# Performance work log

Hardware: AMD Instinct MI355X
Metric: run time of the kernel (lower is better)

## Reference

```python
import jax, jax.numpy as jnp
import numpy as np

B, T, E, H = 2, 2048, 1024, 16
D = E // H
K_KEEP = 391
RECENCY = 64
SCALE = D ** -0.5


def setup_inputs() -> dict:
    key = jax.random.key(0)
    k1, k2, k3 = jax.random.split(key, 3)
    x = jax.random.normal(k1, (B, T, E), jnp.float32)
    W_attn = jax.random.normal(k2, (3 * E, E), jnp.float32) * 0.02  # torch Linear weight [out,in]
    W_proj = jax.random.normal(k3, (E, E), jnp.float32) * 0.02
    return {"x": x, "W_attn": W_attn, "W_proj": W_proj}


def reference(x, W_attn, W_proj):
    b, t, c = x.shape
    qkv = x @ W_attn.T                      # [B,T,3E]
    q, k, v = jnp.split(qkv, 3, axis=-1)
    to_heads = lambda u: u.reshape(b, t, H, D).transpose(0, 2, 1, 3)  # [B,H,T,D]
    q, k, v = to_heads(q), to_heads(k), to_heads(v)

    # first pass: causal attention weights for importance scoring
    scores = jnp.einsum('bhqd,bhkd->bhqk', q, k) * SCALE
    causal = jnp.tril(jnp.ones((t, t), dtype=bool))
    scores = jnp.where(causal, scores, -jnp.inf)
    attn_w = jax.nn.softmax(scores, axis=-1)

    # mean importance over query dim, force-keep recent tokens
    imp = attn_w.mean(axis=2)               # [B,H,T]
    imp = imp.at[:, :, -RECENCY:].set(1.0)

    # top-k token selection per (batch, head)
    _, idx = jax.lax.top_k(imp, K_KEEP)     # [B,H,K]

    # gather pruned K/V
    K_keep = jnp.take_along_axis(k, idx[..., None], axis=2)  # [B,H,K,D]
    V_keep = jnp.take_along_axis(v, idx[..., None], axis=2)

    # second attention pass over pruned keys (no causal mask, matches legacy code)
    s2 = jnp.einsum('bhqd,bhkd->bhqk', q, K_keep) * SCALE
    a2 = jax.nn.softmax(s2, axis=-1)
    out = jnp.einsum('bhqk,bhkd->bhqd', a2, V_keep)          # [B,H,T,D]

    out = out.transpose(0, 2, 1, 3).reshape(b, t, c)
    return out @ W_proj.T
```

## Files before the change

### kernel.cpp

```cpp
#include <hip/hip_runtime.h>
#include <hip/hip_bf16.h>


#define TT 2048
#define EE 1024
#define HH 16
#define DD 64
#define KKEEP 391
#define REC 64
#define NBH 32
#define QSCALE 0.125f
#define KPAD 448

typedef short bf16x8 __attribute__((ext_vector_type(8)));
typedef _Float16 f16x8 __attribute__((ext_vector_type(8)));
typedef float f32x4 __attribute__((ext_vector_type(4)));

static __device__ inline unsigned short bf_rn(float x) {
  unsigned u = __float_as_uint(x);
  unsigned r = u + 0x7fffu + ((u >> 16) & 1u);
  return (unsigned short)(r >> 16);
}
static __device__ inline float bf_up(unsigned short h) {
  return __uint_as_float((unsigned)h << 16);
}
static __device__ inline unsigned pkf16(float a, float b) {
  union { _Float16 h[2]; unsigned u; } t;
  t.h[0] = (_Float16)a; t.h[1] = (_Float16)b; return t.u;
}
static __device__ inline void glds16(const void* g, void* l) {
  __builtin_amdgcn_global_load_lds(
      (const __attribute__((address_space(1))) void*)g,
      (__attribute__((address_space(3))) void*)l, 16, 0, 0);
}

__global__ __launch_bounds__(256) void split_kernel(
    const float* __restrict__ src, unsigned short* __restrict__ ho,
    unsigned short* __restrict__ lo_, int n)
{
  int i = (blockIdx.x * 256 + threadIdx.x) * 4;
  const int stride = gridDim.x * 1024;
  for (; i < n; i += stride) {
    float4 v = *reinterpret_cast<const float4*>(&src[i]);
    ushort4 hh, ll;
    float f;
    hh.x = bf_rn(v.x); f = bf_up(hh.x); ll.x = bf_rn(v.x - f);
    hh.y = bf_rn(v.y); f = bf_up(hh.y); ll.y = bf_rn(v.y - f);
    hh.z = bf_rn(v.z); f = bf_up(hh.z); ll.z = bf_rn(v.z - f);
    hh.w = bf_rn(v.w); f = bf_up(hh.w); ll.w = bf_rn(v.w - f);
    *reinterpret_cast<ushort4*>(&ho[i]) = hh;
    *reinterpret_cast<ushort4*>(&lo_[i]) = ll;
  }
}

__global__ __launch_bounds__(256) void gemm_bf16s_nt(
    const unsigned short* __restrict__ Ah, const unsigned short* __restrict__ Al,
    const unsigned short* __restrict__ Bh, const unsigned short* __restrict__ Bl,
    float* __restrict__ Cc, unsigned short* __restrict__ Qho, unsigned short* __restrict__ Qlo,
    unsigned short* __restrict__ Kho, unsigned short* __restrict__ Klo,
    float* __restrict__ Vo, int M, int N, int Kd, int mode)
{
  __shared__ __align__(16) unsigned short Ahs[2][128 * 32];
  __shared__ __align__(16) unsigned short Als[2][128 * 32];
  __shared__ __align__(16) unsigned short Bhs[2][128 * 32];
  __shared__ __align__(16) unsigned short Bls[2][128 * 32];
  const int tid = threadIdx.x;
  const int m0 = blockIdx.y * 128, n0 = blockIdx.x * 128;
  const int w = tid >> 6, lane = tid & 63;
  const int wm = w >> 1, wn = w & 1;
  const int l15 = lane & 15, l4 = lane >> 4;
  const bool vblk = (mode == 1) && (blockIdx.x >= 16);

  size_t gA[2], gB[2]; int ldso[2];
#pragma unroll
  for (int s = 0; s < 2; s++) {
    int seg = w * 2 + s;
    int r = seg * 16 + (lane >> 2);
    int kb = (lane & 3) ^ ((r >> 1) & 3);
    gA[s] = (size_t)(m0 + r) * Kd + kb * 8;
    gB[s] = (size_t)(n0 + r) * Kd + kb * 8;
    ldso[s] = seg * 512;
  }

  auto STAGE = [&](int bb, int k0) {
#pragma unroll
    for (int s = 0; s < 2; s++) {
      glds16(&Ah[gA[s] + k0], &Ahs[bb][ldso[s]]);
      glds16(&Bh[gB[s] + k0], &Bhs[bb][ldso[s]]);
      if (!vblk) {
        glds16(&Al[gA[s] + k0], &Als[bb][ldso[s]]);
        glds16(&Bl[gB[s] + k0], &Bls[bb][ldso[s]]);
      }
    }
  };

  f32x4 acc[4][4] = {};

  STAGE(0, 0);
  __syncthreads();
  int cur = 0;
  for (int k0 = 0; k0 < Kd; k0 += 32) {
    if (k0 + 32 < Kd) STAGE(cur ^ 1, k0 + 32);
    bf16x8 ah[4], al[4], bh[4], bl[4];
#pragma unroll
    for (int i = 0; i < 4; i++) {
      int ar = wm * 64 + i * 16 + l15;
      int aoff = ar * 32 + ((l4 ^ ((ar >> 1) & 3)) * 8);
      ah[i] = *reinterpret_cast<const bf16x8*>(&Ahs[cur][aoff]);
      int br = wn * 64 + i * 16 + l15;
      int boff = br * 32 + ((l4 ^ ((br >> 1) & 3)) * 8);
      bh[i] = *reinterpret_cast<const bf16x8*>(&Bhs[cur][boff]);
      if (!vblk) {
        al[i] = *reinterpret_cast<const bf16x8*>(&Als[cur][aoff]);
        bl[i] = *reinterpret_cast<const bf16x8*>(&Bls[cur][boff]);
      }
    }
#pragma unroll
    for (int i = 0; i < 4; i++)
#pragma unroll
      for (int j = 0; j < 4; j++) {
        acc[i][j] = __builtin_amdgcn_mfma_f32_16x16x32_bf16(ah[i], bh[j], acc[i][j], 0, 0, 0);
        if (!vblk) {
          acc[i][j] = __builtin_amdgcn_mfma_f32_16x16x32_bf16(ah[i], bl[j], acc[i][j], 0, 0, 0);
          acc[i][j] = __builtin_amdgcn_mfma_f32_16x16x32_bf16(al[i], bh[j], acc[i][j], 0, 0, 0);
        }
      }
    __syncthreads();
    cur ^= 1;
  }

  if (mode == 0) {
#pragma unroll
    for (int i = 0; i < 4; i++) {
      int mrow0 = m0 + wm * 64 + i * 16 + l4 * 4;
#pragma unroll
      for (int j = 0; j < 4; j++) {
        int ncol = n0 + wn * 64 + j * 16 + l15;
#pragma unroll
        for (int r = 0; r < 4; r++)
          Cc[(size_t)(mrow0 + r) * N + ncol] = acc[i][j][r];
      }
    }
  } else {
#pragma unroll
    for (int j = 0; j < 4; j++) {
      int n = n0 + wn * 64 + j * 16 + l15;
      int p = n >> 10, rr = n & 1023;
      int h = rr >> 6, d0 = rr & 63;
#pragma unroll
      for (int i = 0; i < 4; i++) {
        int mrow0 = m0 + wm * 64 + i * 16 + l4 * 4;
#pragma unroll
        for (int r = 0; r < 4; r++) {
          int m = mrow0 + r;
          int b = m >> 11, t = m & 2047;
          size_t idx = ((size_t)((b * HH + h) * TT + t)) * DD + d0;
          float v = acc[i][j][r];
          if (p == 2) {
            Vo[idx] = v;
          } else {
            unsigned short hi_ = bf_rn(v);
            unsigned short lo2 = bf_rn(v - bf_up(hi_));
            if (p == 0) { Qho[idx] = hi_; Qlo[idx] = lo2; }
            else        { Kho[idx] = hi_; Klo[idx] = lo2; }
          }
        }
      }
    }
  }
}

__global__ __launch_bounds__(512) void importance3_kernel(
    const unsigned short* __restrict__ Qh, const unsigned short* __restrict__ Ql,
    const unsigned short* __restrict__ Kh, const unsigned short* __restrict__ Kl,
    float* __restrict__ part)
{
  const int pairid = blockIdx.y, bh = blockIdx.x;
  const int tid = threadIdx.x;
  const int w = tid >> 6, lane = tid & 63;
  const int wm = w >> 1, wn = w & 1;
  const int l15 = lane & 15, l4 = lane >> 4;
  __shared__ __align__(16) unsigned short Qhs[128 * 64];
  __shared__ __align__(16) unsigned short Qls[128 * 64];
  __shared__ __align__(16) unsigned short Khs[2][128 * 64];
  __shared__ __align__(16) unsigned short Kls[2][128 * 64];
  __shared__ float csw[8 * 128];
  __shared__ float rsb[2 * 128];

  int krow[2], kkb[2], klds[2];
#pragma unroll
  for (int s = 0; s < 2; s++) {
    int seg = w * 2 + s;
    int r = seg * 8 + (lane >> 3);
    int k8 = lane & 7;
    krow[s] = r; kkb[s] = k8 ^ (r & 7); klds[s] = seg * 512;
  }
  auto STAGEK = [&](int bb, int ci) {
#pragma unroll
    for (int s = 0; s < 2; s++) {
      size_t ga = ((size_t)(bh * TT + ci * 128 + krow[s])) * DD + kkb[s] * 8;
      glds16(&Kh[ga], &Khs[bb][klds[s]]);
      glds16(&Kl[ga], &Kls[bb][klds[s]]);
    }
  };

  for (int half = 0; half < 2; half++) {
    const int rt = half ? (15 - pairid) : pairid;
    const int row0 = rt * 128;
    const int nch = rt + 1;
    __syncthreads();
#pragma unroll
    for (int cc = 0; cc < 2; cc++) {
      int c = cc * 512 + tid;
      int r = c >> 3, k8 = c & 7;
      int so = r * 64 + ((k8 ^ (r & 7)) * 8);
      size_t ga = ((size_t)(bh * TT + row0 + r)) * DD + k8 * 8;
      *reinterpret_cast<bf16x8*>(&Qhs[so]) = *reinterpret_cast<const bf16x8*>(&Qh[ga]);
      *reinterpret_cast<bf16x8*>(&Qls[so]) = *reinterpret_cast<const bf16x8*>(&Ql[ga]);
    }

    float rsum[2][4];
#pragma unroll
    for (int i = 0; i < 2; i++)
#pragma unroll
      for (int r = 0; r < 4; r++) rsum[i][r] = 0.f;
    float invl[2][4];

    for (int sweep = 0; sweep < 2; sweep++) {
      STAGEK(0, 0);
      __syncthreads();
      int cur = 0;
      for (int ci = 0; ci < nch; ci++) {
        if (ci + 1 < nch) STAGEK(cur ^ 1, ci + 1);
        f32x4 acc[2][4] = {};
#pragma unroll
        for (int ks = 0; ks < 2; ks++) {
          bf16x8 ah[2], al_[2];
#pragma unroll
          for (int i = 0; i < 2; i++) {
            int ar = wm * 32 + i * 16 + l15;
            int off = ar * 64 + (((ks * 4 + l4) ^ (ar & 7)) * 8);
            ah[i]  = *reinterpret_cast<const bf16x8*>(&Qhs[off]);
            al_[i] = *reinterpret_cast<const bf16x8*>(&Qls[off]);
          }
#pragma unroll
          for (int j = 0; j < 4; j++) {
            int br = wn * 64 + j * 16 + l15;
            int off = br * 64 + (((ks * 4 + l4) ^ (br & 7)) * 8);
            bf16x8 bh_ = *reinterpret_cast<const bf16x8*>(&Khs[cur][off]);
            bf16x8 bl_ = *reinterpret_cast<const bf16x8*>(&Kls[cur][off]);
#pragma unroll
            for (int i = 0; i < 2; i++) {
              acc[i][j] = __builtin_amdgcn_mfma_f32_16x16x32_bf16(ah[i], bh_, acc[i][j], 0, 0, 0);
              acc[i][j] = __builtin_amdgcn_mfma_f32_16x16x32_bf16(ah[i], bl_, acc[i][j], 0, 0, 0);
              acc[i][j] = __builtin_amdgcn_mfma_f32_16x16x32_bf16(al_[i], bh_, acc[i][j], 0, 0, 0);
            }
          }
        }
        const bool diag = (ci == rt);
        if (sweep == 0) {
#pragma unroll
          for (int i = 0; i < 2; i++)
#pragma unroll
            for (int r = 0; r < 4; r++) {
              int row = row0 + wm * 32 + i * 16 + l4 * 4 + r;
              float s = 0.f;
#pragma unroll
              for (int j = 0; j < 4; j++) {
                int key = ci * 128 + wn * 64 + j * 16 + l15;
                float p = __expf(acc[i][j][r] * QSCALE);
                if (diag && key > row) p = 0.f;
                s += p;
              }
              rsum[i][r] += s;
            }
          __syncthreads();
        } else {
          float cp[4];
#pragma unroll
          for (int j = 0; j < 4; j++) cp[j] = 0.f;
#pragma unroll
          for (int i = 0; i < 2; i++)
#pragma unroll
            for (int r = 0; r < 4; r++) {
              int row = row0 + wm * 32 + i * 16 + l4 * 4 + r;
              float il = invl[i][r];
#pragma unroll
              for (int j = 0; j < 4; j++) {
                int key = ci * 128 + wn * 64 + j * 16 + l15;
                float p = __expf(acc[i][j][r] * QSCALE) * il;
                if (diag && key > row) p = 0.f;
                cp[j] += p;
              }
            }
#pragma unroll
          for (int j = 0; j < 4; j++) {
            float v = cp[j];
            v += __shfl_xor(v, 16); v += __shfl_xor(v, 32);
            cp[j] = v;
          }
          if (l4 == 0) {
#pragma unroll
            for (int j = 0; j < 4; j++)
              csw[w * 128 + wn * 64 + j * 16 + l15] = cp[j];
          }
          __syncthreads();
          if (tid < 128) {
            int wnc = tid >> 6;
            float s = csw[(0 * 2 + wnc) * 128 + tid] + csw[(1 * 2 + wnc) * 128 + tid] +
                      csw[(2 * 2 + wnc) * 128 + tid] + csw[(3 * 2 + wnc) * 128 + tid];
            size_t pi = ((size_t)(bh * 8 + pairid)) * 2048 + ci * 128 + tid;
            bool wr = (half == 0) || (ci > pairid);
            part[pi] = wr ? s : (part[pi] + s);
          }
          __syncthreads();
        }
        cur ^= 1;
      }
      if (sweep == 0) {
#pragma unroll
        for (int i = 0; i < 2; i++)
#pragma unroll
          for (int r = 0; r < 4; r++) {
            float v = rsum[i][r];
            v += __shfl_xor(v, 1); v += __shfl_xor(v, 2);
            v += __shfl_xor(v, 4); v += __shfl_xor(v, 8);
            rsum[i][r] = v;
          }
        if (l15 == 0) {
#pragma unroll
          for (int i = 0; i < 2; i++)
#pragma unroll
            for (int r = 0; r < 4; r++)
              rsb[wn * 128 + wm * 32 + i * 16 + l4 * 4 + r] = rsum[i][r];
        }
        __syncthreads();
#pragma unroll
        for (int i = 0; i < 2; i++)
#pragma unroll
          for (int r = 0; r < 4; r++) {
            int rl = wm * 32 + i * 16 + l4 * 4 + r;
            invl[i][r] = 1.0f / (rsb[rl] + rsb[128 + rl]);
          }
      }
    }
  }
}

__global__ __launch_bounds__(256) void topk_gather_kernel(
    const float* __restrict__ part,
    const unsigned short* __restrict__ Kh, const unsigned short* __restrict__ Kl,
    const float* __restrict__ V,
    unsigned short* __restrict__ Kf, unsigned short* __restrict__ Vt)
{
  const int bh = blockIdx.x, tid = threadIdx.x;
  const int lane = tid & 63, w = tid >> 6;
  __shared__ int redi[4];
  __shared__ int stot;
  __shared__ int base[256];
  __shared__ int idxb[KKEEP];
  unsigned u[8];
#pragma unroll
  for (int k = 0; k < 8; k++) {
    int e = tid * 8 + k;
    float s = 0.f;
#pragma unroll
    for (int p = 0; p < 8; p++)
      if (e < (16 - p) * 128) s += part[((size_t)(bh * 8 + p)) * 2048 + e];
    float v = (e >= TT - REC) ? 3.0e3f : s;
    u[k] = __float_as_uint(v);
  }
  unsigned lo = 0u, hi = 0x7f800000u;
  for (int it = 0; it < 31; it++) {
    unsigned mid = lo + ((hi - lo + 1) >> 1);
    int c = 0;
#pragma unroll
    for (int k = 0; k < 8; k++) c += (u[k] >= mid) ? 1 : 0;
#pragma unroll
    for (int off = 1; off <= 32; off <<= 1) c += __shfl_xor(c, off);
    if (lane == 0) redi[w] = c;
    __syncthreads();
    int tot = redi[0] + redi[1] + redi[2] + redi[3];
    if (tot >= KKEEP) lo = mid; else hi = mid - 1;
    __syncthreads();
  }
  const unsigned vstar = lo;
  int cgt = 0, ceq = 0;
#pragma unroll
  for (int k = 0; k < 8; k++) { cgt += (u[k] > vstar) ? 1 : 0; ceq += (u[k] == vstar) ? 1 : 0; }
  base[tid] = cgt; __syncthreads();
  if (tid == 0) {
    int run = 0;
    for (int i = 0; i < 256; i++) { int t = base[i]; base[i] = run; run += t; }
    stot = run;
  }
  __syncthreads();
  int off1 = base[tid];
#pragma unroll
  for (int k = 0; k < 8; k++)
    if (u[k] > vstar) idxb[off1++] = tid * 8 + k;
  __syncthreads();
  base[tid] = ceq; __syncthreads();
  if (tid == 0) {
    int run = 0;
    for (int i = 0; i < 256; i++) { int t = base[i]; base[i] = run; run += t; }
  }
  __syncthreads();
  int off2 = stot + base[tid];
#pragma unroll
  for (int k = 0; k < 8; k++)
    if (u[k] == vstar) { if (off2 < KKEEP) idxb[off2] = tid * 8 + k; off2++; }
  __syncthreads();
  for (int f = tid; f < KPAD * 8; f += 256) {
    int kk = f >> 3, c8 = f & 7;
    union { _Float16 h[8]; uint4 v; } o;
#pragma unroll
    for (int j = 0; j < 8; j++) o.h[j] = (_Float16)0.f;
    if (kk < KKEEP) {
      int sr = idxb[kk];
      bf16x8 hv = *reinterpret_cast<const bf16x8*>(&Kh[((size_t)(bh * TT + sr)) * DD + c8 * 8]);
      bf16x8 lv = *reinterpret_cast<const bf16x8*>(&Kl[((size_t)(bh * TT + sr)) * DD + c8 * 8]);
#pragma unroll
      for (int j = 0; j < 8; j++)
        o.h[j] = (_Float16)(bf_up((unsigned short)hv[j]) + bf_up((unsigned short)lv[j]));
    }
    *reinterpret_cast<uint4*>(&Kf[((size_t)(bh * KPAD) + kk) * DD + c8 * 8]) = o.v;
  }
  for (int f = tid; f < KPAD * 8; f += 256) {
    int kk = f >> 3, d8 = f & 7;
    float vv[8];
#pragma unroll
    for (int j = 0; j < 8; j++) vv[j] = 0.f;
    if (kk < KKEEP) {
      int sr = idxb[kk];
      float4 a = *reinterpret_cast<const float4*>(&V[((size_t)(bh * TT + sr)) * DD + d8 * 8]);
      float4 b = *reinterpret_cast<const float4*>(&V[((size_t)(bh * TT + sr)) * DD + d8 * 8 + 4]);
      vv[0] = a.x; vv[1] = a.y; vv[2] = a.z; vv[3] = a.w;
      vv[4] = b.x; vv[5] = b.y; vv[6] = b.z; vv[7] = b.w;
    }
#pragma unroll
    for (int j = 0; j < 8; j++) {
      union { _Float16 h; unsigned short s; } t;
      t.h = (_Float16)vv[j];
      Vt[((size_t)(bh * DD) + d8 * 8 + j) * KPAD + kk] = t.s;
    }
  }
}

__global__ __launch_bounds__(256) void attn3_kernel(
    const unsigned short* __restrict__ Qh, const unsigned short* __restrict__ Ql,
    const unsigned short* __restrict__ Kf, const unsigned short* __restrict__ Vt,
    unsigned short* __restrict__ AOh, unsigned short* __restrict__ AOl)
{
  const int rt = blockIdx.y, bh = blockIdx.x;
  const int tid = threadIdx.x;
  const int w = tid >> 6, lane = tid & 63;
  const int l15 = lane & 15, l4 = lane >> 4;
  __shared__ __align__(16) unsigned short Qs[64 * 64];
  __shared__ __align__(16) unsigned short Ks[2][64 * 64];
  __shared__ __align__(16) unsigned short Vs[2][64 * 64];
  __shared__ float LDSo[4][64][16];
  const int row0 = rt * 64;

  int srow[2], skb[2], slds[2];
#pragma unroll
  for (int s = 0; s < 2; s++) {
    int seg = w * 2 + s;
    int r = seg * 8 + (lane >> 3);
    int k8 = lane & 7;
    srow[s] = r; skb[s] = k8 ^ (r & 7); slds[s] = seg * 512;
  }
  auto STAGEA = [&](int bb, int ci) {
#pragma unroll
    for (int s = 0; s < 2; s++) {
      glds16(&Kf[((size_t)(bh * KPAD) + ci * 64 + srow[s]) * DD + skb[s] * 8], &Ks[bb][slds[s]]);
      glds16(&Vt[((size_t)(bh * DD) + srow[s]) * KPAD + ci * 64 + skb[s] * 8], &Vs[bb][slds[s]]);
    }
  };

#pragma unroll
  for (int it = 0; it < 2; it++) {
    int idx = it * 256 + tid;
    int r = idx >> 3, k8 = idx & 7;
    size_t ga = ((size_t)(bh * TT + row0 + r)) * DD + k8 * 8;
    bf16x8 hv = *reinterpret_cast<const bf16x8*>(&Qh[ga]);
    bf16x8 lv = *reinterpret_cast<const bf16x8*>(&Ql[ga]);
    union { _Float16 h[8]; uint4 v; } q16;
#pragma unroll
    for (int j = 0; j < 8; j++)
      q16.h[j] = (_Float16)(bf_up((unsigned short)hv[j]) + bf_up((unsigned short)lv[j]));
    *reinterpret_cast<uint4*>(&Qs[r * 64 + ((k8 ^ (r & 7)) * 8)]) = q16.v;
  }
  STAGEA(0, 0);
  __syncthreads();
  f16x8 bq[2];
#pragma unroll
  for (int ks = 0; ks < 2; ks++) {
    int br = w * 16 + l15;
    bq[ks] = *reinterpret_cast<const f16x8*>(&Qs[br * 64 + (((ks * 4 + l4) ^ (br & 7)) * 8)]);
  }

  f32x4 acc_o[4] = {};
  float rsum = 0.f;
  int cur = 0;

  for (int ci = 0; ci < 7; ci++) {
    if (ci + 1 < 7) STAGEA(cur ^ 1, ci + 1);
    f32x4 accs[4] = {};
#pragma unroll
    for (int ks = 0; ks < 2; ks++) {
#pragma unroll
      for (int i = 0; i < 4; i++) {
        int kr = i * 16 + l15;
        f16x8 af = *reinterpret_cast<const f16x8*>(&Ks[cur][kr * 64 + (((ks * 4 + l4) ^ (kr & 7)) * 8)]);
        accs[i] = __builtin_amdgcn_mfma_f32_16x16x32_f16(af, bq[ks], accs[i], 0, 0, 0);
      }
    }
    float p[4][4];
#pragma unroll
    for (int i = 0; i < 4; i++)
#pragma unroll
      for (int r = 0; r < 4; r++) {
        int gk = ci * 64 + i * 16 + l4 * 4 + r;
        float pp = __expf(accs[i][r] * QSCALE);
        if (gk >= KKEEP) pp = 0.f;
        p[i][r] = pp;
        rsum += pp;
      }
    unsigned pkU[4][2];
#pragma unroll
    for (int i = 0; i < 4; i++) {
      pkU[i][0] = pkf16(p[i][0], p[i][1]);
      pkU[i][1] = pkf16(p[i][2], p[i][3]);
    }
#pragma unroll
    for (int ks = 0; ks < 2; ks++) {
      union { f16x8 h; unsigned u[4]; } bp;
#pragma unroll
      for (int wp = 0; wp < 4; wp++) {
        int src = ((l4 & 1) * 2 + (wp >> 1)) * 16 + l15;
        unsigned v0 = (unsigned)__shfl((int)pkU[ks * 2][wp & 1], src);
        unsigned v1 = (unsigned)__shfl((int)pkU[ks * 2 + 1][wp & 1], src);
        bp.u[wp] = (l4 & 2) ? v1 : v0;
      }
#pragma unroll
      for (int i = 0; i < 4; i++) {
        int dr = i * 16 + l15;
        f16x8 av = *reinterpret_cast<const f16x8*>(&Vs[cur][dr * 64 + (((ks * 4 + l4) ^ (dr & 7)) * 8)]);
        acc_o[i] = __builtin_amdgcn_mfma_f32_16x16x32_f16(av, bp.h, acc_o[i], 0, 0, 0);
      }
    }
    __syncthreads();
    cur ^= 1;
  }
  rsum += __shfl_xor(rsum, 16);
  rsum += __shfl_xor(rsum, 32);
  float inv = 1.0f / rsum;
#pragma unroll
  for (int i = 0; i < 4; i++)
#pragma unroll
    for (int r = 0; r < 4; r++)
      LDSo[w][i * 16 + l4 * 4 + r][l15] = acc_o[i][r] * inv;
  __syncthreads();
  const int b = bh >> 4, h = bh & 15;
#pragma unroll
  for (int uu = 0; uu < 2; uu++) {
    int u = uu * 64 + lane;
    int q = u >> 3, dc = u & 7;
    int row = row0 + w * 16 + q;
    union { unsigned short s[8]; uint4 v; } sh, sl;
#pragma unroll
    for (int j = 0; j < 8; j++) {
      float v = LDSo[w][dc * 8 + j][q];
      unsigned short hh = bf_rn(v);
      sh.s[j] = hh;
      sl.s[j] = bf_rn(v - bf_up(hh));
    }
    size_t addr = ((size_t)(b * TT + row)) * EE + h * DD + dc * 8;
    *reinterpret_cast<uint4*>(&AOh[addr]) = sh.v;
    *reinterpret_cast<uint4*>(&AOl[addr]) = sl.v;
  }
}

extern "C" void kernel_launch(void* const* d_in, const int* in_sizes, int n_in,
                              void* d_out, int out_size, void* d_ws, size_t ws_size,
                              hipStream_t stream)
{
  const float* x     = (const float*)d_in[0];
  const float* Wattn = (const float*)d_in[1];
  const float* Wproj = (const float*)d_in[2];
  float* out = (float*)d_out;
  float* ws  = (float*)d_ws;

  const size_t SZQ = (size_t)NBH * TT * DD;
  const size_t SZK = (size_t)NBH * KPAD * DD;
  float* Vb   = ws;
  float* part = Vb + SZQ;
  unsigned short* Kf  = (unsigned short*)(part + (size_t)NBH * 8 * TT);
  unsigned short* Vt  = Kf + SZK;
  unsigned short* Qhp = Vt + SZK;
  unsigned short* Qlp = Qhp + SZQ;
  unsigned short* Khp = Qlp + SZQ;
  unsigned short* Klp = Khp + SZQ;
  unsigned short* xh  = Klp + SZQ;
  unsigned short* xl  = xh + (size_t)4096 * 1024;
  unsigned short* Wh  = xl + (size_t)4096 * 1024;
  unsigned short* Wl  = Wh + (size_t)3072 * 1024;
  unsigned short* AOh = xh;
  unsigned short* AOl = xl;
  unsigned short* Ph  = Wh;
  unsigned short* Pl  = Ph + (size_t)1024 * 1024;

  const size_t needB =
      ((size_t)SZQ + (size_t)NBH * 8 * TT) * 4 +
      ((size_t)2 * SZK + (size_t)4 * SZQ + (size_t)2 * 4096 * 1024 + (size_t)2 * 3072 * 1024) * 2;
  if (ws_size < needB) return;

  split_kernel<<<512, 256, 0, stream>>>(x, xh, xl, 4096 * 1024);
  split_kernel<<<512, 256, 0, stream>>>(Wattn, Wh, Wl, 3072 * 1024);
  gemm_bf16s_nt<<<dim3(24, 32), 256, 0, stream>>>(xh, xl, Wh, Wl, nullptr,
                                                  Qhp, Qlp, Khp, Klp, Vb, 4096, 3072, 1024, 1);
  split_kernel<<<512, 256, 0, stream>>>(Wproj, Ph, Pl, 1024 * 1024);
  importance3_kernel<<<dim3(NBH, 8), 512, 0, stream>>>(Qhp, Qlp, Khp, Klp, part);
  topk_gather_kernel<<<NBH, 256, 0, stream>>>(part, Khp, Klp, Vb, Kf, Vt);
  attn3_kernel<<<dim3(NBH, 32), 256, 0, stream>>>(Qhp, Qlp, Kf, Vt, AOh, AOl);
  gemm_bf16s_nt<<<dim3(8, 32), 256, 0, stream>>>(AOh, AOl, Ph, Pl, out,
                                                 nullptr, nullptr, nullptr, nullptr, nullptr,
                                                 4096, 1024, 1024, 0);
}
```

Before: 313.3 us.

## Deepen async-copy pipelines, split QKV GEMM by V precision, fuse split launches

```diff
diff --git a/kernel.cpp b/kernel.cpp
--- a/kernel.cpp
+++ b/kernel.cpp
@@ -16,6 +16,10 @@
 typedef _Float16 f16x8 __attribute__((ext_vector_type(8)));
 typedef float f32x4 __attribute__((ext_vector_type(4)));
 
+#define WAIT_VM(N) asm volatile("s_waitcnt vmcnt(" #N ")" ::: "memory")
+#define WAIT_LGKM0 asm volatile("s_waitcnt lgkmcnt(0)" ::: "memory")
+#define BAR() __builtin_amdgcn_s_barrier()
+
 static __device__ inline unsigned short bf_rn(float x) {
   unsigned u = __float_as_uint(x);
   unsigned r = u + 0x7fffu + ((u >> 16) & 1u);
@@ -34,42 +38,61 @@
       (__attribute__((address_space(3))) void*)l, 16, 0, 0);
 }
 
+static __device__ inline void split4(const float* __restrict__ src,
+                                     unsigned short* __restrict__ ho,
+                                     unsigned short* __restrict__ lo_, int i)
+{
+  float4 v = *reinterpret_cast<const float4*>(&src[i]);
+  ushort4 hh, ll;
+  float f;
+  hh.x = bf_rn(v.x); f = bf_up(hh.x); ll.x = bf_rn(v.x - f);
+  hh.y = bf_rn(v.y); f = bf_up(hh.y); ll.y = bf_rn(v.y - f);
+  hh.z = bf_rn(v.z); f = bf_up(hh.z); ll.z = bf_rn(v.z - f);
+  hh.w = bf_rn(v.w); f = bf_up(hh.w); ll.w = bf_rn(v.w - f);
+  *reinterpret_cast<ushort4*>(&ho[i]) = hh;
+  *reinterpret_cast<ushort4*>(&lo_[i]) = ll;
+}
+
 __global__ __launch_bounds__(256) void split_kernel(
     const float* __restrict__ src, unsigned short* __restrict__ ho,
     unsigned short* __restrict__ lo_, int n)
 {
   int i = (blockIdx.x * 256 + threadIdx.x) * 4;
   const int stride = gridDim.x * 1024;
-  for (; i < n; i += stride) {
-    float4 v = *reinterpret_cast<const float4*>(&src[i]);
-    ushort4 hh, ll;
-    float f;
-    hh.x = bf_rn(v.x); f = bf_up(hh.x); ll.x = bf_rn(v.x - f);
-    hh.y = bf_rn(v.y); f = bf_up(hh.y); ll.y = bf_rn(v.y - f);
-    hh.z = bf_rn(v.z); f = bf_up(hh.z); ll.z = bf_rn(v.z - f);
-    hh.w = bf_rn(v.w); f = bf_up(hh.w); ll.w = bf_rn(v.w - f);
-    *reinterpret_cast<ushort4*>(&ho[i]) = hh;
-    *reinterpret_cast<ushort4*>(&lo_[i]) = ll;
-  }
-}
-
-__global__ __launch_bounds__(256) void gemm_bf16s_nt(
+  for (; i < n; i += stride) split4(src, ho, lo_, i);
+}
+
+__global__ __launch_bounds__(256) void split2_kernel(
+    const float* __restrict__ x, const float* __restrict__ wa,
+    unsigned short* __restrict__ xh, unsigned short* __restrict__ xl,
+    unsigned short* __restrict__ wh, unsigned short* __restrict__ wl)
+{
+  const int n1 = 4096 * 1024, n2 = 3072 * 1024;
+  int i = (blockIdx.x * 256 + threadIdx.x) * 4;
+  const int stride = gridDim.x * 1024;
+  for (; i < n1 + n2; i += stride) {
+    if (i < n1) split4(x, xh, xl, i);
+    else        split4(wa, wh, wl, i - n1);
+  }
+}
+
+template<bool VB, int MODE>
+__global__ __launch_bounds__(256) void gemm_pipe(
     const unsigned short* __restrict__ Ah, const unsigned short* __restrict__ Al,
     const unsigned short* __restrict__ Bh, const unsigned short* __restrict__ Bl,
     float* __restrict__ Cc, unsigned short* __restrict__ Qho, unsigned short* __restrict__ Qlo,
     unsigned short* __restrict__ Kho, unsigned short* __restrict__ Klo,
-    float* __restrict__ Vo, int M, int N, int Kd, int mode)
+    float* __restrict__ Vo, int M, int N, int Kd, int nOff)
 {
   __shared__ __align__(16) unsigned short Ahs[2][128 * 32];
-  __shared__ __align__(16) unsigned short Als[2][128 * 32];
   __shared__ __align__(16) unsigned short Bhs[2][128 * 32];
-  __shared__ __align__(16) unsigned short Bls[2][128 * 32];
+  __shared__ __align__(16) unsigned short Als[VB ? 1 : 2][128 * 32];
+  __shared__ __align__(16) unsigned short Bls[VB ? 1 : 2][128 * 32];
   const int tid = threadIdx.x;
-  const int m0 = blockIdx.y * 128, n0 = blockIdx.x * 128;
+  const int m0 = blockIdx.y * 128, n0 = nOff + blockIdx.x * 128;
   const int w = tid >> 6, lane = tid & 63;
   const int wm = w >> 1, wn = w & 1;
   const int l15 = lane & 15, l4 = lane >> 4;
-  const bool vblk = (mode == 1) && (blockIdx.x >= 16);
 
   size_t gA[2], gB[2]; int ldso[2];
 #pragma unroll
@@ -81,13 +104,12 @@
     gB[s] = (size_t)(n0 + r) * Kd + kb * 8;
     ldso[s] = seg * 512;
   }
-
   auto STAGE = [&](int bb, int k0) {
 #pragma unroll
     for (int s = 0; s < 2; s++) {
       glds16(&Ah[gA[s] + k0], &Ahs[bb][ldso[s]]);
       glds16(&Bh[gB[s] + k0], &Bhs[bb][ldso[s]]);
-      if (!vblk) {
+      if (!VB) {
         glds16(&Al[gA[s] + k0], &Als[bb][ldso[s]]);
         glds16(&Bl[gB[s] + k0], &Bls[bb][ldso[s]]);
       }
@@ -97,10 +119,12 @@
   f32x4 acc[4][4] = {};
 
   STAGE(0, 0);
-  __syncthreads();
+  STAGE(1, 32);
   int cur = 0;
   for (int k0 = 0; k0 < Kd; k0 += 32) {
-    if (k0 + 32 < Kd) STAGE(cur ^ 1, k0 + 32);
+    if (k0 + 32 < Kd) { if (VB) WAIT_VM(4); else WAIT_VM(8); }
+    else WAIT_VM(0);
+    BAR();
     bf16x8 ah[4], al[4], bh[4], bl[4];
 #pragma unroll
     for (int i = 0; i < 4; i++) {
@@ -110,7 +134,7 @@
       int br = wn * 64 + i * 16 + l15;
       int boff = br * 32 + ((l4 ^ ((br >> 1) & 3)) * 8);
       bh[i] = *reinterpret_cast<const bf16x8*>(&Bhs[cur][boff]);
-      if (!vblk) {
+      if (!VB) {
         al[i] = *reinterpret_cast<const bf16x8*>(&Als[cur][aoff]);
         bl[i] = *reinterpret_cast<const bf16x8*>(&Bls[cur][boff]);
       }
@@ -120,16 +144,18 @@
 #pragma unroll
       for (int j = 0; j < 4; j++) {
         acc[i][j] = __builtin_amdgcn_mfma_f32_16x16x32_bf16(ah[i], bh[j], acc[i][j], 0, 0, 0);
-        if (!vblk) {
+        if (!VB) {
           acc[i][j] = __builtin_amdgcn_mfma_f32_16x16x32_bf16(ah[i], bl[j], acc[i][j], 0, 0, 0);
           acc[i][j] = __builtin_amdgcn_mfma_f32_16x16x32_bf16(al[i], bh[j], acc[i][j], 0, 0, 0);
         }
       }
-    __syncthreads();
+    WAIT_LGKM0;
+    BAR();
+    if (k0 + 64 < Kd) STAGE(cur, k0 + 64);
     cur ^= 1;
   }
 
-  if (mode == 0) {
+  if (MODE == 0) {
 #pragma unroll
     for (int i = 0; i < 4; i++) {
       int mrow0 = m0 + wm * 64 + i * 16 + l4 * 4;
@@ -139,6 +165,23 @@
 #pragma unroll
         for (int r = 0; r < 4; r++)
           Cc[(size_t)(mrow0 + r) * N + ncol] = acc[i][j][r];
+      }
+    }
+  } else if (VB) {
+#pragma unroll
+    for (int j = 0; j < 4; j++) {
+      int n = n0 + wn * 64 + j * 16 + l15;
+      int rr = n & 1023;
+      int h = rr >> 6, d0 = rr & 63;
+#pragma unroll
+      for (int i = 0; i < 4; i++) {
+        int mrow0 = m0 + wm * 64 + i * 16 + l4 * 4;
+#pragma unroll
+        for (int r = 0; r < 4; r++) {
+          int m = mrow0 + r;
+          int b = m >> 11, t = m & 2047;
+          Vo[((size_t)((b * HH + h) * TT + t)) * DD + d0] = acc[i][j][r];
+        }
       }
     }
   } else {
@@ -156,21 +199,17 @@
           int b = m >> 11, t = m & 2047;
           size_t idx = ((size_t)((b * HH + h) * TT + t)) * DD + d0;
           float v = acc[i][j][r];
-          if (p == 2) {
-            Vo[idx] = v;
-          } else {
-            unsigned short hi_ = bf_rn(v);
-            unsigned short lo2 = bf_rn(v - bf_up(hi_));
-            if (p == 0) { Qho[idx] = hi_; Qlo[idx] = lo2; }
-            else        { Kho[idx] = hi_; Klo[idx] = lo2; }
-          }
+          unsigned short hi_ = bf_rn(v);
+          unsigned short lo2 = bf_rn(v - bf_up(hi_));
+          if (p == 0) { Qho[idx] = hi_; Qlo[idx] = lo2; }
+          else        { Kho[idx] = hi_; Klo[idx] = lo2; }
         }
       }
     }
   }
 }
 
-__global__ __launch_bounds__(512) void importance3_kernel(
+__global__ __launch_bounds__(512) void importance4_kernel(
     const unsigned short* __restrict__ Qh, const unsigned short* __restrict__ Ql,
     const unsigned short* __restrict__ Kh, const unsigned short* __restrict__ Kl,
     float* __restrict__ part)
@@ -218,6 +257,17 @@
       *reinterpret_cast<bf16x8*>(&Qhs[so]) = *reinterpret_cast<const bf16x8*>(&Qh[ga]);
       *reinterpret_cast<bf16x8*>(&Qls[so]) = *reinterpret_cast<const bf16x8*>(&Ql[ga]);
     }
+    __syncthreads();
+    bf16x8 aq[2][2], aql[2][2];
+#pragma unroll
+    for (int ks = 0; ks < 2; ks++)
+#pragma unroll
+      for (int i = 0; i < 2; i++) {
+        int ar = wm * 32 + i * 16 + l15;
+        int off = ar * 64 + (((ks * 4 + l4) ^ (ar & 7)) * 8);
+        aq[ks][i]  = *reinterpret_cast<const bf16x8*>(&Qhs[off]);
+        aql[ks][i] = *reinterpret_cast<const bf16x8*>(&Qls[off]);
+      }
 
     float rsum[2][4];
 #pragma unroll
@@ -228,21 +278,14 @@
 
     for (int sweep = 0; sweep < 2; sweep++) {
       STAGEK(0, 0);
-      __syncthreads();
+      if (nch > 1) STAGEK(1, 1);
       int cur = 0;
       for (int ci = 0; ci < nch; ci++) {
-        if (ci + 1 < nch) STAGEK(cur ^ 1, ci + 1);
+        if (ci + 1 < nch) WAIT_VM(4); else WAIT_VM(0);
+        BAR();
         f32x4 acc[2][4] = {};
 #pragma unroll
         for (int ks = 0; ks < 2; ks++) {
-          bf16x8 ah[2], al_[2];
-#pragma unroll
-          for (int i = 0; i < 2; i++) {
-            int ar = wm * 32 + i * 16 + l15;
-            int off = ar * 64 + (((ks * 4 + l4) ^ (ar & 7)) * 8);
-            ah[i]  = *reinterpret_cast<const bf16x8*>(&Qhs[off]);
-            al_[i] = *reinterpret_cast<const bf16x8*>(&Qls[off]);
-          }
 #pragma unroll
           for (int j = 0; j < 4; j++) {
             int br = wn * 64 + j * 16 + l15;
@@ -251,9 +294,9 @@
             bf16x8 bl_ = *reinterpret_cast<const bf16x8*>(&Kls[cur][off]);
 #pragma unroll
             for (int i = 0; i < 2; i++) {
-              acc[i][j] = __builtin_amdgcn_mfma_f32_16x16x32_bf16(ah[i], bh_, acc[i][j], 0, 0, 0);
-              acc[i][j] = __builtin_amdgcn_mfma_f32_16x16x32_bf16(ah[i], bl_, acc[i][j], 0, 0, 0);
-              acc[i][j] = __builtin_amdgcn_mfma_f32_16x16x32_bf16(al_[i], bh_, acc[i][j], 0, 0, 0);
+              acc[i][j] = __builtin_amdgcn_mfma_f32_16x16x32_bf16(aq[ks][i], bh_, acc[i][j], 0, 0, 0);
+              acc[i][j] = __builtin_amdgcn_mfma_f32_16x16x32_bf16(aq[ks][i], bl_, acc[i][j], 0, 0, 0);
+              acc[i][j] = __builtin_amdgcn_mfma_f32_16x16x32_bf16(aql[ks][i], bh_, acc[i][j], 0, 0, 0);
             }
           }
         }
@@ -274,7 +317,9 @@
               }
               rsum[i][r] += s;
             }
-          __syncthreads();
+          WAIT_LGKM0;
+          BAR();
+          if (ci + 2 < nch) STAGEK(cur, ci + 2);
         } else {
           float cp[4];
 #pragma unroll
@@ -299,12 +344,16 @@
             v += __shfl_xor(v, 16); v += __shfl_xor(v, 32);
             cp[j] = v;
           }
+          WAIT_LGKM0;
+          BAR();
+          if (ci + 2 < nch) STAGEK(cur, ci + 2);
           if (l4 == 0) {
 #pragma unroll
             for (int j = 0; j < 4; j++)
               csw[w * 128 + wn * 64 + j * 16 + l15] = cp[j];
           }
-          __syncthreads();
+          WAIT_LGKM0;
+          BAR();
           if (tid < 128) {
             int wnc = tid >> 6;
             float s = csw[(0 * 2 + wnc) * 128 + tid] + csw[(1 * 2 + wnc) * 128 + tid] +
@@ -313,7 +362,6 @@
             bool wr = (half == 0) || (ci > pairid);
             part[pi] = wr ? s : (part[pi] + s);
           }
-          __syncthreads();
         }
         cur ^= 1;
       }
@@ -327,6 +375,7 @@
             v += __shfl_xor(v, 4); v += __shfl_xor(v, 8);
             rsum[i][r] = v;
           }
+        __syncthreads();
         if (l15 == 0) {
 #pragma unroll
           for (int i = 0; i < 2; i++)
@@ -447,7 +496,7 @@
   }
 }
 
-__global__ __launch_bounds__(256) void attn3_kernel(
+__global__ __launch_bounds__(256) void attn4_kernel(
     const unsigned short* __restrict__ Qh, const unsigned short* __restrict__ Ql,
     const unsigned short* __restrict__ Kf, const unsigned short* __restrict__ Vt,
     unsigned short* __restrict__ AOh, unsigned short* __restrict__ AOl)
@@ -492,7 +541,9 @@
     *reinterpret_cast<uint4*>(&Qs[r * 64 + ((k8 ^ (r & 7)) * 8)]) = q16.v;
   }
   STAGEA(0, 0);
-  __syncthreads();
+  STAGEA(1, 1);
+  WAIT_LGKM0;
+  BAR();
   f16x8 bq[2];
 #pragma unroll
   for (int ks = 0; ks < 2; ks++) {
@@ -505,7 +556,8 @@
   int cur = 0;
 
   for (int ci = 0; ci < 7; ci++) {
-    if (ci + 1 < 7) STAGEA(cur ^ 1, ci + 1);
+    if (ci + 1 < 7) WAIT_VM(4); else WAIT_VM(0);
+    BAR();
     f32x4 accs[4] = {};
 #pragma unroll
     for (int ks = 0; ks < 2; ks++) {
@@ -550,7 +602,9 @@
         acc_o[i] = __builtin_amdgcn_mfma_f32_16x16x32_f16(av, bp.h, acc_o[i], 0, 0, 0);
       }
     }
-    __syncthreads();
+    WAIT_LGKM0;
+    BAR();
+    if (ci + 2 < 7) STAGEA(cur, ci + 2);
     cur ^= 1;
   }
   rsum += __shfl_xor(rsum, 16);
@@ -616,15 +670,15 @@
       ((size_t)2 * SZK + (size_t)4 * SZQ + (size_t)2 * 4096 * 1024 + (size_t)2 * 3072 * 1024) * 2;
   if (ws_size < needB) return;
 
-  split_kernel<<<512, 256, 0, stream>>>(x, xh, xl, 4096 * 1024);
-  split_kernel<<<512, 256, 0, stream>>>(Wattn, Wh, Wl, 3072 * 1024);
-  gemm_bf16s_nt<<<dim3(24, 32), 256, 0, stream>>>(xh, xl, Wh, Wl, nullptr,
-                                                  Qhp, Qlp, Khp, Klp, Vb, 4096, 3072, 1024, 1);
-  split_kernel<<<512, 256, 0, stream>>>(Wproj, Ph, Pl, 1024 * 1024);
-  importance3_kernel<<<dim3(NBH, 8), 512, 0, stream>>>(Qhp, Qlp, Khp, Klp, part);
+  split2_kernel<<<1024, 256, 0, stream>>>(x, Wattn, xh, xl, Wh, Wl);
+  gemm_pipe<false, 1><<<dim3(16, 32), 256, 0, stream>>>(xh, xl, Wh, Wl, nullptr,
+      Qhp, Qlp, Khp, Klp, nullptr, 4096, 3072, 1024, 0);
+  gemm_pipe<true, 1><<<dim3(8, 32), 256, 0, stream>>>(xh, xl, Wh, Wl, nullptr,
+      nullptr, nullptr, nullptr, nullptr, Vb, 4096, 3072, 1024, 2048);
+  split_kernel<<<256, 256, 0, stream>>>(Wproj, Ph, Pl, 1024 * 1024);
+  importance4_kernel<<<dim3(NBH, 8), 512, 0, stream>>>(Qhp, Qlp, Khp, Klp, part);
   topk_gather_kernel<<<NBH, 256, 0, stream>>>(part, Khp, Klp, Vb, Kf, Vt);
-  attn3_kernel<<<dim3(NBH, 32), 256, 0, stream>>>(Qhp, Qlp, Kf, Vt, AOh, AOl);
-  gemm_bf16s_nt<<<dim3(8, 32), 256, 0, stream>>>(AOh, AOl, Ph, Pl, out,
-                                                 nullptr, nullptr, nullptr, nullptr, nullptr,
-                                                 4096, 1024, 1024, 0);
-}
+  attn4_kernel<<<dim3(NBH, 32), 256, 0, stream>>>(Qhp, Qlp, Kf, Vt, AOh, AOl);
+  gemm_pipe<false, 0><<<dim3(8, 32), 256, 0, stream>>>(AOh, AOl, Ph, Pl, out,
+      nullptr, nullptr, nullptr, nullptr, nullptr, 4096, 1024, 1024, 0);
+}
```

Measured after the change: 265.0 us. -15.4%, faster.
